# Kernel optimization log

Hardware: AMD Instinct MI355X
Metric: run time of the kernel (lower is better)

The kernel has to match this reference:

```python
import jax, jax.numpy as jnp
import numpy as np

B, C, H, W = 8, 64, 64, 64
IC = max(1, C // 8)  # inter_channels


def setup_inputs() -> dict:
    key = jax.random.key(0)
    ks = jax.random.split(key, 8)
    return {
        "x": jax.random.normal(ks[0], (B, C, H, W), dtype=jnp.float32),
        "theta_w": jax.random.normal(ks[1], (IC, C), dtype=jnp.float32) * 0.05,
        "theta_b": jnp.zeros((IC,), dtype=jnp.float32),
        "phi_w": jax.random.normal(ks[2], (IC, C), dtype=jnp.float32) * 0.05,
        "phi_b": jnp.zeros((IC,), dtype=jnp.float32),
        "g_w": jax.random.normal(ks[3], (C, C), dtype=jnp.float32) * 0.05,
        "g_b": jnp.zeros((C,), dtype=jnp.float32),
        "gamma": jax.random.normal(ks[4], (1,), dtype=jnp.float32),
    }


def reference(x, theta_w, theta_b, phi_w, phi_b, g_w, g_b, gamma):
    b, c, h, w = x.shape
    n = h * w
    xf = x.reshape(b, c, n)  # flatten spatial
    # 1x1 convs == per-pixel channel matmuls
    theta = jnp.einsum('ic,bcn->bin', theta_w, xf) + theta_b[None, :, None]  # [b, IC, n]
    phi = jnp.einsum('ic,bcn->bin', phi_w, xf) + phi_b[None, :, None]        # [b, IC, n]
    g = jnp.einsum('oc,bcn->bon', g_w, xf) + g_b[None, :, None]              # [b, C, n]
    # attn[b, q, k] = theta_q . phi_k, softmax over keys
    attn = jax.nn.softmax(jnp.einsum('biq,bik->bqk', theta, phi), axis=-1)   # [b, n, n]
    # out = g @ attn^T  (torch: bmm(g, attn.transpose(1,2)))
    out = jnp.einsum('bck,bqk->bcq', g, attn).reshape(b, c, h, w)
    return x + gamma[0] * out
```

## Files before the change

### kernel.cpp

```cpp
#include <hip/hip_runtime.h>
#include <cstddef>
#include <cstdint>


#define Bb 8
#define Cc 64
#define NN 4096
#define IC 8
#define VSTR 72
#define XSTR 72

typedef __attribute__((ext_vector_type(8)))  short bf16x8;
typedef __attribute__((ext_vector_type(16))) float f32x16;
typedef unsigned short ushort_t;
typedef unsigned int   uint_t;

#define LOG2E 1.4426950408889634f

static __device__ __forceinline__ uint_t f2bf(float x) {
    union { float f; uint_t u; } v; v.f = x;
    uint_t r = v.u + 0x7FFF + ((v.u >> 16) & 1);
    return r >> 16;
}
static __device__ __forceinline__ float bf2f(ushort_t u) {
    union { uint_t u; float f; } v; v.u = ((uint_t)u) << 16;
    return v.f;
}
static __device__ __forceinline__ float fexp2(float x) {
#if __has_builtin(__builtin_amdgcn_exp2f)
    return __builtin_amdgcn_exp2f(x);
#else
    return exp2f(x);
#endif
}
static __device__ __forceinline__ uint_t fbits(float x) {
    union { float f; uint_t u; } v; v.f = x; return v.u;
}
static __device__ __forceinline__ uint_t packbf(float e, float o) {
#if __has_builtin(__builtin_amdgcn_perm)
    return __builtin_amdgcn_perm(fbits(o), fbits(e), 0x07060302u);
#else
    return (fbits(e) >> 16) | (fbits(o) & 0xFFFF0000u);
#endif
}

union U4B { uint4 u; bf16x8 v; };

__global__ __launch_bounds__(256) void p1_kernel(
    const float* __restrict__ x,
    const float* __restrict__ theta_w, const float* __restrict__ theta_b,
    const float* __restrict__ phi_w,   const float* __restrict__ phi_b,
    const float* __restrict__ g_w,     const float* __restrict__ g_b,
    ushort_t* __restrict__ xbf, ushort_t* __restrict__ Wbf, float* __restrict__ biasf)
{
    const int t = threadIdx.x;
    const int bid = blockIdx.x;
    if (bid < 512) {
        __shared__ float Xt[64 * 68];
        const int b  = bid >> 6;
        const int nt = (bid & 63) * 64;
        const int c = t >> 2, nsg = t & 3;
        const float* xs = x + ((size_t)(b * 64 + c)) * NN + nt + nsg * 16;
        #pragma unroll
        for (int i = 0; i < 4; i++) {
            float4 v = ((const float4*)xs)[i];
            *(float4*)(Xt + c * 68 + nsg * 16 + i * 4) = v;
        }
        __syncthreads();
        const int n = t & 63, cs = t >> 6;
        uint_t wv[8];
        #pragma unroll
        for (int i = 0; i < 8; i++) {
            float e0 = Xt[(cs * 16 + 2 * i + 0) * 68 + n];
            float e1 = Xt[(cs * 16 + 2 * i + 1) * 68 + n];
            wv[i] = f2bf(e0) | (f2bf(e1) << 16);
        }
        ushort_t* dst = xbf + ((size_t)(b * NN + nt + n)) * 64 + cs * 16;
        *(uint4*)dst       = make_uint4(wv[0], wv[1], wv[2], wv[3]);
        *(uint4*)(dst + 8) = make_uint4(wv[4], wv[5], wv[6], wv[7]);
    } else {
        for (int i = t; i < 96 * 64; i += 256) {
            int row = i >> 6, c = i & 63;
            float v;
            if (row < 64)      v = g_w[row * 64 + c];
            else if (row < 72) v = theta_w[(row - 64) * 64 + c] * LOG2E;
            else if (row < 80) v = phi_w[(row - 72) * 64 + c];
            else               v = 0.0f;
            Wbf[i] = (ushort_t)f2bf(v);
        }
        if (t < 96) {
            float bv = (t < 64) ? g_b[t]
                     : (t < 72) ? theta_b[t - 64] * LOG2E
                     : (t < 80) ? phi_b[t - 72] : 0.0f;
            biasf[t] = bv;
        }
    }
}

__global__ __launch_bounds__(256) void p2_kernel(
    const ushort_t* __restrict__ xbf, const ushort_t* __restrict__ Wbf,
    const float* __restrict__ biasf,
    ushort_t* __restrict__ Qw, ushort_t* __restrict__ Kw, ushort_t* __restrict__ Vt)
{
    __shared__ ushort_t Xs[128 * XSTR];
    __shared__ float bs[96];

    const int t = threadIdx.x;
    const int lane = t & 63, w = t >> 6;
    const int l31 = lane & 31, hi = lane >> 5;
    const int b  = blockIdx.x >> 5;
    const int n0 = (blockIdx.x & 31) * 128;

    {
        const int n = t >> 1, h = t & 1;
        const ushort_t* src = xbf + ((size_t)(b * NN + n0 + n)) * 64 + h * 32;
        #pragma unroll
        for (int i = 0; i < 4; i++) {
            uint4 v = ((const uint4*)src)[i];
            *(uint4*)(Xs + n * XSTR + h * 32 + i * 8) = v;
        }
    }
    if (t < 96) bs[t] = biasf[t];
    __syncthreads();

    bf16x8 af[3][4];
    #pragma unroll
    for (int mt = 0; mt < 3; mt++)
        #pragma unroll
        for (int kc = 0; kc < 4; kc++)
            af[mt][kc] = *(const bf16x8*)(Wbf + (size_t)(mt * 32 + l31) * 64 + kc * 16 + hi * 8);

    f32x16 ac0 = {}, ac1 = {}, ac2 = {};
    #pragma unroll
    for (int kc = 0; kc < 4; kc++) {
        bf16x8 bv = *(const bf16x8*)(Xs + (w * 32 + l31) * XSTR + kc * 16 + hi * 8);
        ac0 = __builtin_amdgcn_mfma_f32_32x32x16_bf16(af[0][kc], bv, ac0, 0, 0, 0);
        ac1 = __builtin_amdgcn_mfma_f32_32x32x16_bf16(af[1][kc], bv, ac1, 0, 0, 0);
        ac2 = __builtin_amdgcn_mfma_f32_32x32x16_bf16(af[2][kc], bv, ac2, 0, 0, 0);
    }

    const int nw = n0 + w * 32;
    const int sig = ((l31 >> 3) & 1) * 16 + ((l31 >> 2) & 1) * 8 + ((l31 >> 4) & 1) * 4 + (l31 & 3);

    #pragma unroll
    for (int reg = 0; reg < 16; reg++) {
        int m = reg >> 2, r = reg & 3;
        {
            int ch = 4 * hi + 8 * m + r;
            float val = ac0[reg] + bs[ch];
            Vt[((size_t)(b * 64 + ch)) * NN + nw + sig] = (ushort_t)f2bf(val);
        }
        {
            int ch = 32 + 4 * hi + 8 * m + r;
            float val = ac1[reg] + bs[ch];
            Vt[((size_t)(b * 64 + ch)) * NN + nw + sig] = (ushort_t)f2bf(val);
        }
    }
    {
        float q0 = ac2[0] + bs[64 + 4 * hi + 0];
        float q1 = ac2[1] + bs[64 + 4 * hi + 1];
        float q2 = ac2[2] + bs[64 + 4 * hi + 2];
        float q3 = ac2[3] + bs[64 + 4 * hi + 3];
        uint2 qp = make_uint2(f2bf(q0) | (f2bf(q1) << 16), f2bf(q2) | (f2bf(q3) << 16));
        *(uint2*)(Qw + ((size_t)(b * NN) + nw + l31) * 8 + hi * 4) = qp;
        float p0 = ac2[4] + bs[72 + 4 * hi + 0];
        float p1 = ac2[5] + bs[72 + 4 * hi + 1];
        float p2 = ac2[6] + bs[72 + 4 * hi + 2];
        float p3 = ac2[7] + bs[72 + 4 * hi + 3];
        uint2 kp = make_uint2(f2bf(p0) | (f2bf(p1) << 16), f2bf(p2) | (f2bf(p3) << 16));
        *(uint2*)(Kw + ((size_t)(b * NN) + nw + l31) * 8 + hi * 4) = kp;
    }
}

template <int FIN>
__global__ __launch_bounds__(256) void attn_kernel(
    const ushort_t* __restrict__ Qw, const ushort_t* __restrict__ Kw,
    const ushort_t* __restrict__ Vt,
    ushort_t* __restrict__ P, float* __restrict__ L, int nsplit,
    const float* __restrict__ x, const float* __restrict__ gamma,
    float* __restrict__ out)
{
    __shared__ ushort_t Vs[64 * VSTR];

    const int t = threadIdx.x;
    const int lane = t & 63, w = t >> 6;
    const int l31 = lane & 31, hi = lane >> 5;

    int bid = blockIdx.x;
    const int qt = bid & 31;
    const int b  = (bid >> 5) & 7;
    const int s  = bid >> 8;
    const int q0 = qt * 128 + w * 32;
    const int keys = NN / nsplit;
    const int k0 = s * keys;
    const int ntiles = keys / 64;

    const ushort_t* Kb = Kw + (size_t)b * NN * 8;
    const ushort_t* Vb = Vt + (size_t)b * 64 * NN;

    bf16x8 qf = {};
    if (hi == 0)
        qf = *(const bf16x8*)(Qw + ((size_t)b * NN + q0 + l31) * 8);

    const int vch = t >> 2, vsg = t & 3;
    const ushort_t* vsrc = Vb + (size_t)vch * NN + k0 + vsg * 16;

    uint4 vc0 = *(const uint4*)(vsrc);
    uint4 vc1 = *(const uint4*)(vsrc + 8);
    uint4 kc0 = {}, kc1 = {};
    if (hi == 0) {
        kc0 = *(const uint4*)(Kb + (size_t)(k0 + l31) * 8);
        kc1 = *(const uint4*)(Kb + (size_t)(k0 + 32 + l31) * 8);
    }

    f32x16 acc0 = {}, acc1 = {};
    float lsum = 0.0f;
    const f32x16 zf = {};

    for (int tt = 0; tt < ntiles; ++tt) {
        __syncthreads();
        *(uint4*)(Vs + vch * VSTR + vsg * 16)     = vc0;
        *(uint4*)(Vs + vch * VSTR + vsg * 16 + 8) = vc1;
        __syncthreads();

        uint4 vn0 = {}, vn1 = {}, kn0 = {}, kn1 = {};
        if (tt + 1 < ntiles) {
            const ushort_t* vs2 = vsrc + (size_t)(tt + 1) * 64;
            vn0 = *(const uint4*)(vs2);
            vn1 = *(const uint4*)(vs2 + 8);
            if (hi == 0) {
                kn0 = *(const uint4*)(Kb + (size_t)(k0 + (tt + 1) * 64 + l31) * 8);
                kn1 = *(const uint4*)(Kb + (size_t)(k0 + (tt + 1) * 64 + 32 + l31) * 8);
            }
        }

        U4B ka0, ka1; ka0.u = kc0; ka1.u = kc1;
        f32x16 S0 = __builtin_amdgcn_mfma_f32_32x32x16_bf16(ka0.v, qf, zf, 0, 0, 0);
        f32x16 S1 = __builtin_amdgcn_mfma_f32_32x32x16_bf16(ka1.v, qf, zf, 0, 0, 0);

        float p0[16], p1[16];
        #pragma unroll
        for (int i = 0; i < 16; i++) { p0[i] = fexp2(S0[i]); }
        #pragma unroll
        for (int i = 0; i < 16; i++) { p1[i] = fexp2(S1[i]); }
        #pragma unroll
        for (int i = 0; i < 16; i++) { lsum += p0[i]; lsum += p1[i]; }

        uint_t pk0[8], pk1[8];
        #pragma unroll
        for (int m = 0; m < 4; m++) {
            #pragma unroll
            for (int rp = 0; rp < 2; rp++) {
                pk0[m * 2 + rp] = packbf(p0[m * 4 + 2 * rp], p0[m * 4 + 2 * rp + 1]);
                pk1[m * 2 + rp] = packbf(p1[m * 4 + 2 * rp], p1[m * 4 + 2 * rp + 1]);
            }
        }

        #pragma unroll
        for (int kf = 0; kf < 2; kf++) {
            #pragma unroll
            for (int c = 0; c < 2; c++) {
                U4B bu;
                if (kf == 0) bu.u = make_uint4(pk0[c * 2], pk0[c * 2 + 1], pk0[(c + 2) * 2], pk0[(c + 2) * 2 + 1]);
                else         bu.u = make_uint4(pk1[c * 2], pk1[c * 2 + 1], pk1[(c + 2) * 2], pk1[(c + 2) * 2 + 1]);
                bf16x8 av0 = *(const bf16x8*)(Vs + (0 * 32 + l31) * VSTR + kf * 32 + c * 16 + hi * 8);
                bf16x8 av1 = *(const bf16x8*)(Vs + (1 * 32 + l31) * VSTR + kf * 32 + c * 16 + hi * 8);
                acc0 = __builtin_amdgcn_mfma_f32_32x32x16_bf16(av0, bu.v, acc0, 0, 0, 0);
                acc1 = __builtin_amdgcn_mfma_f32_32x32x16_bf16(av1, bu.v, acc1, 0, 0, 0);
            }
        }

        vc0 = vn0; vc1 = vn1; kc0 = kn0; kc1 = kn1;
    }

    float ltot = lsum + __shfl_xor(lsum, 32);

    if (!FIN) {
        ushort_t* Pb = P + ((size_t)(s * Bb + b) * 64) * NN;
        #pragma unroll
        for (int reg = 0; reg < 16; reg++) {
            int m = reg >> 2, r = reg & 3;
            int ch0 = 4 * hi + 8 * m + r;
            Pb[(size_t)ch0 * NN + q0 + l31]        = (ushort_t)f2bf(acc0[reg]);
            Pb[(size_t)(ch0 + 32) * NN + q0 + l31] = (ushort_t)f2bf(acc1[reg]);
        }
        if (lane < 32)
            L[(size_t)(s * Bb + b) * NN + q0 + lane] = ltot;
    } else {
        const float gm = gamma[0];
        const float inv = 1.0f / ltot;
        #pragma unroll
        for (int reg = 0; reg < 16; reg++) {
            int m = reg >> 2, r = reg & 3;
            int ch0 = 4 * hi + 8 * m + r;
            size_t i0 = ((size_t)(b * 64 + ch0)) * NN + q0 + l31;
            size_t i1 = ((size_t)(b * 64 + ch0 + 32)) * NN + q0 + l31;
            out[i0] = x[i0] + gm * acc0[reg] * inv;
            out[i1] = x[i1] + gm * acc1[reg] * inv;
        }
    }
}

__global__ __launch_bounds__(256) void combine_kernel(
    const ushort_t* __restrict__ P, const float* __restrict__ L,
    const float* __restrict__ x, const float* __restrict__ gamma,
    float* __restrict__ out, int nsplit)
{
    const int T = blockIdx.x * 256 + threadIdx.x;
    const int q = T & (NN - 1);
    const int r2 = T >> 12;
    const int b = r2 & 7;
    const int cg = r2 >> 3;

    float ls = 0.0f;
    for (int s = 0; s < nsplit; s++)
        ls += L[(size_t)(s * Bb + b) * NN + q];

    float a[16];
    #pragma unroll
    for (int j = 0; j < 16; j++) a[j] = 0.0f;
    for (int s = 0; s < nsplit; s++) {
        const ushort_t* Pb = P + ((size_t)(s * Bb + b) * 64 + cg * 16) * NN + q;
        #pragma unroll
        for (int j = 0; j < 16; j++)
            a[j] += bf2f(Pb[(size_t)j * NN]);
    }

    const float inv = 1.0f / ls;
    const float gm = gamma[0];
    #pragma unroll
    for (int j = 0; j < 16; j++) {
        size_t idx = ((size_t)(b * 64 + cg * 16 + j)) * NN + q;
        out[idx] = x[idx] + gm * a[j] * inv;
    }
}

extern "C" void kernel_launch(void* const* d_in, const int* in_sizes, int n_in,
                              void* d_out, int out_size, void* d_ws, size_t ws_size,
                              hipStream_t stream)
{
    const float* x       = (const float*)d_in[0];
    const float* theta_w = (const float*)d_in[1];
    const float* theta_b = (const float*)d_in[2];
    const float* phi_w   = (const float*)d_in[3];
    const float* phi_b   = (const float*)d_in[4];
    const float* g_w     = (const float*)d_in[5];
    const float* g_b     = (const float*)d_in[6];
    const float* gamma   = (const float*)d_in[7];
    float* out = (float*)d_out;

    char* p = (char*)d_ws;
    ushort_t* Qw  = (ushort_t*)p;  p += (size_t)Bb * NN * 8 * 2;
    ushort_t* Kw  = (ushort_t*)p;  p += (size_t)Bb * NN * 8 * 2;
    ushort_t* Vt  = (ushort_t*)p;  p += (size_t)Bb * 64 * NN * 2;
    ushort_t* xbf = (ushort_t*)p;  p += (size_t)Bb * NN * 64 * 2;
    ushort_t* Wbf = (ushort_t*)p;  p += 96 * 64 * 2;
    float*    biasf = (float*)p;   p += 96 * 4 + 128;
    char*     pbase = p;
    const size_t base_bytes  = (size_t)(pbase - (char*)d_ws);
    const size_t split_bytes = (size_t)Bb * 64 * NN * 2 + (size_t)Bb * NN * 4;

    int ns = 1;
    const int cands[3] = {4, 2, 1};
    for (int i = 0; i < 3; i++)
        if (base_bytes + (size_t)cands[i] * split_bytes <= ws_size) { ns = cands[i]; break; }

    ushort_t* P = (ushort_t*)pbase;
    float*    L = (float*)(pbase + (size_t)ns * Bb * 64 * NN * 2);

    p1_kernel<<<513, 256, 0, stream>>>(x, theta_w, theta_b, phi_w, phi_b, g_w, g_b,
                                       xbf, Wbf, biasf);
    p2_kernel<<<Bb * 32, 256, 0, stream>>>(xbf, Wbf, biasf, Qw, Kw, Vt);

    if (ns > 1) {
        attn_kernel<0><<<ns * Bb * 32, 256, 0, stream>>>(Qw, Kw, Vt, P, L, ns,
                                                         nullptr, nullptr, nullptr);
        combine_kernel<<<(Bb * NN * 4) / 256, 256, 0, stream>>>(P, L, x, gamma, out, ns);
    } else {
        attn_kernel<1><<<Bb * 32, 256, 0, stream>>>(Qw, Kw, Vt, P, L, 1, x, gamma, out);
    }
}
```

Before: 57.94 us.

## Double-buffer V tiles with 128-key steps and vectorize combine kernel

The attention kernel now processes 128 keys per iteration, keeps two LDS buffers for V, and prefetches two tiles ahead. This cuts the barriers per tile from two to one and lets global loads overlap the MFMA work. The split count becomes a template parameter so the loop bounds are fixed at compile time. The combine kernel handles 8 queries per thread with 16-byte loads and stores, and its grid shrinks to 128 blocks. This costs more LDS and registers per block, and the smaller combine grid may not fill the GPU.

```diff
diff --git a/kernel.cpp b/kernel.cpp
--- a/kernel.cpp
+++ b/kernel.cpp
@@ -7,7 +7,7 @@
 #define Cc 64
 #define NN 4096
 #define IC 8
-#define VSTR 72
+#define VSTR 136
 #define XSTR 72
 
 typedef __attribute__((ext_vector_type(8)))  short bf16x8;
@@ -22,9 +22,8 @@
     uint_t r = v.u + 0x7FFF + ((v.u >> 16) & 1);
     return r >> 16;
 }
-static __device__ __forceinline__ float bf2f(ushort_t u) {
-    union { uint_t u; float f; } v; v.u = ((uint_t)u) << 16;
-    return v.f;
+static __device__ __forceinline__ float bitsf(uint_t u) {
+    union { uint_t u; float f; } v; v.u = u; return v.f;
 }
 static __device__ __forceinline__ float fexp2(float x) {
 #if __has_builtin(__builtin_amdgcn_exp2f)
@@ -172,15 +171,17 @@
     }
 }
 
-template <int FIN>
+template <int FIN, int NSPLIT>
 __global__ __launch_bounds__(256) void attn_kernel(
     const ushort_t* __restrict__ Qw, const ushort_t* __restrict__ Kw,
     const ushort_t* __restrict__ Vt,
-    ushort_t* __restrict__ P, float* __restrict__ L, int nsplit,
+    ushort_t* __restrict__ P, float* __restrict__ L,
     const float* __restrict__ x, const float* __restrict__ gamma,
     float* __restrict__ out)
 {
-    __shared__ ushort_t Vs[64 * VSTR];
+    constexpr int KEYS = NN / NSPLIT;
+    constexpr int NT = KEYS / 128;
+    __shared__ ushort_t Vs[2][64][VSTR];
 
     const int t = threadIdx.x;
     const int lane = t & 63, w = t >> 6;
@@ -191,9 +192,7 @@
     const int b  = (bid >> 5) & 7;
     const int s  = bid >> 8;
     const int q0 = qt * 128 + w * 32;
-    const int keys = NN / nsplit;
-    const int k0 = s * keys;
-    const int ntiles = keys / 64;
+    const int k0 = s * KEYS;
 
     const ushort_t* Kb = Kw + (size_t)b * NN * 8;
     const ushort_t* Vb = Vt + (size_t)b * 64 * NN;
@@ -203,74 +202,108 @@
         qf = *(const bf16x8*)(Qw + ((size_t)b * NN + q0 + l31) * 8);
 
     const int vch = t >> 2, vsg = t & 3;
-    const ushort_t* vsrc = Vb + (size_t)vch * NN + k0 + vsg * 16;
-
-    uint4 vc0 = *(const uint4*)(vsrc);
-    uint4 vc1 = *(const uint4*)(vsrc + 8);
-    uint4 kc0 = {}, kc1 = {};
+    const ushort_t* vsrc = Vb + (size_t)vch * NN + k0 + vsg * 32;
+
+    uint4 vA[4];
+    uint4 kcur[4] = {make_uint4(0,0,0,0), make_uint4(0,0,0,0),
+                     make_uint4(0,0,0,0), make_uint4(0,0,0,0)};
+    uint4 kA[4]   = {make_uint4(0,0,0,0), make_uint4(0,0,0,0),
+                     make_uint4(0,0,0,0), make_uint4(0,0,0,0)};
+
+    #pragma unroll
+    for (int i = 0; i < 4; i++) vA[i] = *(const uint4*)(vsrc + i * 8);
     if (hi == 0) {
-        kc0 = *(const uint4*)(Kb + (size_t)(k0 + l31) * 8);
-        kc1 = *(const uint4*)(Kb + (size_t)(k0 + 32 + l31) * 8);
-    }
+        #pragma unroll
+        for (int kf = 0; kf < 4; kf++)
+            kcur[kf] = *(const uint4*)(Kb + (size_t)(k0 + kf * 32 + l31) * 8);
+    }
+    #pragma unroll
+    for (int i = 0; i < 4; i++)
+        *(uint4*)(&Vs[0][vch][vsg * 32 + i * 8]) = vA[i];
+    if (NT > 1) {
+        #pragma unroll
+        for (int i = 0; i < 4; i++) vA[i] = *(const uint4*)(vsrc + 128 + i * 8);
+        if (hi == 0) {
+            #pragma unroll
+            for (int kf = 0; kf < 4; kf++)
+                kA[kf] = *(const uint4*)(Kb + (size_t)(k0 + 128 + kf * 32 + l31) * 8);
+        }
+    }
+    __syncthreads();
 
     f32x16 acc0 = {}, acc1 = {};
     float lsum = 0.0f;
     const f32x16 zf = {};
 
-    for (int tt = 0; tt < ntiles; ++tt) {
+    for (int tt = 0; tt < NT; ++tt) {
+        const int cur = tt & 1;
+        if (tt + 1 < NT) {
+            #pragma unroll
+            for (int i = 0; i < 4; i++)
+                *(uint4*)(&Vs[cur ^ 1][vch][vsg * 32 + i * 8]) = vA[i];
+        }
+        if (tt + 2 < NT) {
+            const ushort_t* v2 = vsrc + (size_t)(tt + 2) * 128;
+            #pragma unroll
+            for (int i = 0; i < 4; i++) vA[i] = *(const uint4*)(v2 + i * 8);
+        }
+
+        #pragma unroll
+        for (int ks = 0; ks < 2; ks++) {
+            U4B ka0, ka1;
+            ka0.u = kcur[2 * ks];
+            ka1.u = kcur[2 * ks + 1];
+            f32x16 S0 = __builtin_amdgcn_mfma_f32_32x32x16_bf16(ka0.v, qf, zf, 0, 0, 0);
+            f32x16 S1 = __builtin_amdgcn_mfma_f32_32x32x16_bf16(ka1.v, qf, zf, 0, 0, 0);
+
+            float p0[16], p1[16];
+            #pragma unroll
+            for (int i = 0; i < 16; i++) p0[i] = fexp2(S0[i]);
+            #pragma unroll
+            for (int i = 0; i < 16; i++) p1[i] = fexp2(S1[i]);
+            #pragma unroll
+            for (int i = 0; i < 16; i++) { lsum += p0[i]; lsum += p1[i]; }
+
+            uint_t pk0[8], pk1[8];
+            #pragma unroll
+            for (int m = 0; m < 4; m++) {
+                #pragma unroll
+                for (int rp = 0; rp < 2; rp++) {
+                    pk0[m * 2 + rp] = packbf(p0[m * 4 + 2 * rp], p0[m * 4 + 2 * rp + 1]);
+                    pk1[m * 2 + rp] = packbf(p1[m * 4 + 2 * rp], p1[m * 4 + 2 * rp + 1]);
+                }
+            }
+
+            #pragma unroll
+            for (int kf = 0; kf < 2; kf++) {
+                #pragma unroll
+                for (int c = 0; c < 2; c++) {
+                    U4B bu;
+                    if (kf == 0) bu.u = make_uint4(pk0[c * 2], pk0[c * 2 + 1],
+                                                   pk0[(c + 2) * 2], pk0[(c + 2) * 2 + 1]);
+                    else         bu.u = make_uint4(pk1[c * 2], pk1[c * 2 + 1],
+                                                   pk1[(c + 2) * 2], pk1[(c + 2) * 2 + 1]);
+                    bf16x8 av0 = *(const bf16x8*)(&Vs[cur][0 * 32 + l31][ks * 64 + kf * 32 + c * 16 + hi * 8]);
+                    bf16x8 av1 = *(const bf16x8*)(&Vs[cur][1 * 32 + l31][ks * 64 + kf * 32 + c * 16 + hi * 8]);
+                    acc0 = __builtin_amdgcn_mfma_f32_32x32x16_bf16(av0, bu.v, acc0, 0, 0, 0);
+                    acc1 = __builtin_amdgcn_mfma_f32_32x32x16_bf16(av1, bu.v, acc1, 0, 0, 0);
+                }
+            }
+        }
+
+        if (tt + 1 < NT) {
+            #pragma unroll
+            for (int kf = 0; kf < 4; kf++) kcur[kf] = kA[kf];
+        }
+        if (tt + 2 < NT) {
+            if (hi == 0) {
+                const ushort_t* kk2 = Kb + (size_t)(k0 + (tt + 2) * 128) * 8;
+                #pragma unroll
+                for (int kf = 0; kf < 4; kf++)
+                    kA[kf] = *(const uint4*)(kk2 + (size_t)(kf * 32 + l31) * 8);
+            }
+        }
         __syncthreads();
-        *(uint4*)(Vs + vch * VSTR + vsg * 16)     = vc0;
-        *(uint4*)(Vs + vch * VSTR + vsg * 16 + 8) = vc1;
-        __syncthreads();
-
-        uint4 vn0 = {}, vn1 = {}, kn0 = {}, kn1 = {};
-        if (tt + 1 < ntiles) {
-            const ushort_t* vs2 = vsrc + (size_t)(tt + 1) * 64;
-            vn0 = *(const uint4*)(vs2);
-            vn1 = *(const uint4*)(vs2 + 8);
-            if (hi == 0) {
-                kn0 = *(const uint4*)(Kb + (size_t)(k0 + (tt + 1) * 64 + l31) * 8);
-                kn1 = *(const uint4*)(Kb + (size_t)(k0 + (tt + 1) * 64 + 32 + l31) * 8);
-            }
-        }
-
-        U4B ka0, ka1; ka0.u = kc0; ka1.u = kc1;
-        f32x16 S0 = __builtin_amdgcn_mfma_f32_32x32x16_bf16(ka0.v, qf, zf, 0, 0, 0);
-        f32x16 S1 = __builtin_amdgcn_mfma_f32_32x32x16_bf16(ka1.v, qf, zf, 0, 0, 0);
-
-        float p0[16], p1[16];
-        #pragma unroll
-        for (int i = 0; i < 16; i++) { p0[i] = fexp2(S0[i]); }
-        #pragma unroll
-        for (int i = 0; i < 16; i++) { p1[i] = fexp2(S1[i]); }
-        #pragma unroll
-        for (int i = 0; i < 16; i++) { lsum += p0[i]; lsum += p1[i]; }
-
-        uint_t pk0[8], pk1[8];
-        #pragma unroll
-        for (int m = 0; m < 4; m++) {
-            #pragma unroll
-            for (int rp = 0; rp < 2; rp++) {
-                pk0[m * 2 + rp] = packbf(p0[m * 4 + 2 * rp], p0[m * 4 + 2 * rp + 1]);
-                pk1[m * 2 + rp] = packbf(p1[m * 4 + 2 * rp], p1[m * 4 + 2 * rp + 1]);
-            }
-        }
-
-        #pragma unroll
-        for (int kf = 0; kf < 2; kf++) {
-            #pragma unroll
-            for (int c = 0; c < 2; c++) {
-                U4B bu;
-                if (kf == 0) bu.u = make_uint4(pk0[c * 2], pk0[c * 2 + 1], pk0[(c + 2) * 2], pk0[(c + 2) * 2 + 1]);
-                else         bu.u = make_uint4(pk1[c * 2], pk1[c * 2 + 1], pk1[(c + 2) * 2], pk1[(c + 2) * 2 + 1]);
-                bf16x8 av0 = *(const bf16x8*)(Vs + (0 * 32 + l31) * VSTR + kf * 32 + c * 16 + hi * 8);
-                bf16x8 av1 = *(const bf16x8*)(Vs + (1 * 32 + l31) * VSTR + kf * 32 + c * 16 + hi * 8);
-                acc0 = __builtin_amdgcn_mfma_f32_32x32x16_bf16(av0, bu.v, acc0, 0, 0, 0);
-                acc1 = __builtin_amdgcn_mfma_f32_32x32x16_bf16(av1, bu.v, acc1, 0, 0, 0);
-            }
-        }
-
-        vc0 = vn0; vc1 = vn1; kc0 = kn0; kc1 = kn1;
     }
 
     float ltot = lsum + __shfl_xor(lsum, 32);
@@ -306,32 +339,64 @@
     const float* __restrict__ x, const float* __restrict__ gamma,
     float* __restrict__ out, int nsplit)
 {
-    const int T = blockIdx.x * 256 + threadIdx.x;
-    const int q = T & (NN - 1);
-    const int r2 = T >> 12;
-    const int b = r2 & 7;
-    const int cg = r2 >> 3;
-
-    float ls = 0.0f;
-    for (int s = 0; s < nsplit; s++)
-        ls += L[(size_t)(s * Bb + b) * NN + q];
-
-    float a[16];
-    #pragma unroll
-    for (int j = 0; j < 16; j++) a[j] = 0.0f;
+    const int g = blockIdx.x * 256 + threadIdx.x;
+    const int qo = g & 511;
+    const int q0 = qo * 8;
+    const int rest = g >> 9;
+    const int b  = rest & 7;
+    const int cg = rest >> 3;
+
+    float ls[8];
+    #pragma unroll
+    for (int j = 0; j < 8; j++) ls[j] = 0.f;
     for (int s = 0; s < nsplit; s++) {
-        const ushort_t* Pb = P + ((size_t)(s * Bb + b) * 64 + cg * 16) * NN + q;
-        #pragma unroll
-        for (int j = 0; j < 16; j++)
-            a[j] += bf2f(Pb[(size_t)j * NN]);
-    }
-
-    const float inv = 1.0f / ls;
+        const float* Lb = L + (size_t)(s * Bb + b) * NN + q0;
+        float4 l0 = *(const float4*)(Lb);
+        float4 l1 = *(const float4*)(Lb + 4);
+        ls[0] += l0.x; ls[1] += l0.y; ls[2] += l0.z; ls[3] += l0.w;
+        ls[4] += l1.x; ls[5] += l1.y; ls[6] += l1.z; ls[7] += l1.w;
+    }
+
+    float a[8][8];
+    #pragma unroll
+    for (int j = 0; j < 8; j++)
+        #pragma unroll
+        for (int k = 0; k < 8; k++) a[j][k] = 0.f;
+
+    for (int s = 0; s < nsplit; s++) {
+        #pragma unroll
+        for (int j = 0; j < 8; j++) {
+            const ushort_t* Pr = P + ((size_t)(s * Bb + b) * 64 + cg * 8 + j) * NN + q0;
+            uint4 pv = *(const uint4*)Pr;
+            uint_t u0 = pv.x, u1 = pv.y, u2 = pv.z, u3 = pv.w;
+            a[j][0] += bitsf(u0 << 16); a[j][1] += bitsf(u0 & 0xFFFF0000u);
+            a[j][2] += bitsf(u1 << 16); a[j][3] += bitsf(u1 & 0xFFFF0000u);
+            a[j][4] += bitsf(u2 << 16); a[j][5] += bitsf(u2 & 0xFFFF0000u);
+            a[j][6] += bitsf(u3 << 16); a[j][7] += bitsf(u3 & 0xFFFF0000u);
+        }
+    }
+
+    float inv[8];
+    #pragma unroll
+    for (int k = 0; k < 8; k++) inv[k] = 1.0f / ls[k];
     const float gm = gamma[0];
-    #pragma unroll
-    for (int j = 0; j < 16; j++) {
-        size_t idx = ((size_t)(b * 64 + cg * 16 + j)) * NN + q;
-        out[idx] = x[idx] + gm * a[j] * inv;
+
+    #pragma unroll
+    for (int j = 0; j < 8; j++) {
+        const size_t ro = ((size_t)(b * 64 + cg * 8 + j)) * NN + q0;
+        float4 x0 = *(const float4*)(x + ro);
+        float4 x1 = *(const float4*)(x + ro + 4);
+        float4 o0, o1;
+        o0.x = x0.x + gm * a[j][0] * inv[0];
+        o0.y = x0.y + gm * a[j][1] * inv[1];
+        o0.z = x0.z + gm * a[j][2] * inv[2];
+        o0.w = x0.w + gm * a[j][3] * inv[3];
+        o1.x = x1.x + gm * a[j][4] * inv[4];
+        o1.y = x1.y + gm * a[j][5] * inv[5];
+        o1.z = x1.z + gm * a[j][6] * inv[6];
+        o1.w = x1.w + gm * a[j][7] * inv[7];
+        *(float4*)(out + ro)     = o0;
+        *(float4*)(out + ro + 4) = o1;
     }
 }
 
@@ -372,11 +437,16 @@
                                        xbf, Wbf, biasf);
     p2_kernel<<<Bb * 32, 256, 0, stream>>>(xbf, Wbf, biasf, Qw, Kw, Vt);
 
-    if (ns > 1) {
-        attn_kernel<0><<<ns * Bb * 32, 256, 0, stream>>>(Qw, Kw, Vt, P, L, ns,
-                                                         nullptr, nullptr, nullptr);
-        combine_kernel<<<(Bb * NN * 4) / 256, 256, 0, stream>>>(P, L, x, gamma, out, ns);
+    if (ns == 4) {
+        attn_kernel<0, 4><<<4 * Bb * 32, 256, 0, stream>>>(Qw, Kw, Vt, P, L,
+                                                           x, gamma, out);
+        combine_kernel<<<128, 256, 0, stream>>>(P, L, x, gamma, out, 4);
+    } else if (ns == 2) {
+        attn_kernel<0, 2><<<2 * Bb * 32, 256, 0, stream>>>(Qw, Kw, Vt, P, L,
+                                                           x, gamma, out);
+        combine_kernel<<<128, 256, 0, stream>>>(P, L, x, gamma, out, 2);
     } else {
-        attn_kernel<1><<<Bb * 32, 256, 0, stream>>>(Qw, Kw, Vt, P, L, 1, x, gamma, out);
-    }
-}
+        attn_kernel<1, 1><<<Bb * 32, 256, 0, stream>>>(Qw, Kw, Vt, P, L,
+                                                       x, gamma, out);
+    }
+}
```

Result: slower. 106.0 us (+82.9%).

## Swizzle V shared tile, vectorize combine, allow 8-way key split

Applied to the files above, without the earlier changes.

Replaces the padded V tile in LDS with an XOR-swizzled 64-wide layout, which reduces LDS footprint and aims to avoid bank conflicts on the MFMA operand reads. The combine kernel is reworked so each thread handles 8 consecutive queries across 8 channels, using 16-byte loads and stores for partial sums, normalizers, x and out. The split candidates now include 8, so more attention blocks can run when workspace allows, at the cost of more partial-result traffic in the combine step.

```diff
diff --git a/kernel.cpp b/kernel.cpp
--- a/kernel.cpp
+++ b/kernel.cpp
@@ -7,7 +7,6 @@
 #define Cc 64
 #define NN 4096
 #define IC 8
-#define VSTR 72
 #define XSTR 72
 
 typedef __attribute__((ext_vector_type(8)))  short bf16x8;
@@ -16,15 +15,15 @@
 typedef unsigned int   uint_t;
 
 #define LOG2E 1.4426950408889634f
+#define VIDX(row, slot) (((row) << 6) + (((slot) ^ ((row) & 7)) << 3))
 
 static __device__ __forceinline__ uint_t f2bf(float x) {
     union { float f; uint_t u; } v; v.f = x;
     uint_t r = v.u + 0x7FFF + ((v.u >> 16) & 1);
     return r >> 16;
 }
-static __device__ __forceinline__ float bf2f(ushort_t u) {
-    union { uint_t u; float f; } v; v.u = ((uint_t)u) << 16;
-    return v.f;
+static __device__ __forceinline__ float bitsf(uint_t u) {
+    union { uint_t u; float f; } v; v.u = u; return v.f;
 }
 static __device__ __forceinline__ float fexp2(float x) {
 #if __has_builtin(__builtin_amdgcn_exp2f)
@@ -180,7 +179,7 @@
     const float* __restrict__ x, const float* __restrict__ gamma,
     float* __restrict__ out)
 {
-    __shared__ ushort_t Vs[64 * VSTR];
+    __shared__ ushort_t Vs[64 * 64];
 
     const int t = threadIdx.x;
     const int lane = t & 63, w = t >> 6;
@@ -204,6 +203,8 @@
 
     const int vch = t >> 2, vsg = t & 3;
     const ushort_t* vsrc = Vb + (size_t)vch * NN + k0 + vsg * 16;
+    const int ws0 = VIDX(vch, 2 * vsg);
+    const int ws1 = VIDX(vch, 2 * vsg + 1);
 
     uint4 vc0 = *(const uint4*)(vsrc);
     uint4 vc1 = *(const uint4*)(vsrc + 8);
@@ -219,8 +220,8 @@
 
     for (int tt = 0; tt < ntiles; ++tt) {
         __syncthreads();
-        *(uint4*)(Vs + vch * VSTR + vsg * 16)     = vc0;
-        *(uint4*)(Vs + vch * VSTR + vsg * 16 + 8) = vc1;
+        *(uint4*)(Vs + ws0) = vc0;
+        *(uint4*)(Vs + ws1) = vc1;
         __syncthreads();
 
         uint4 vn0 = {}, vn1 = {}, kn0 = {}, kn1 = {};
@@ -263,8 +264,9 @@
                 U4B bu;
                 if (kf == 0) bu.u = make_uint4(pk0[c * 2], pk0[c * 2 + 1], pk0[(c + 2) * 2], pk0[(c + 2) * 2 + 1]);
                 else         bu.u = make_uint4(pk1[c * 2], pk1[c * 2 + 1], pk1[(c + 2) * 2], pk1[(c + 2) * 2 + 1]);
-                bf16x8 av0 = *(const bf16x8*)(Vs + (0 * 32 + l31) * VSTR + kf * 32 + c * 16 + hi * 8);
-                bf16x8 av1 = *(const bf16x8*)(Vs + (1 * 32 + l31) * VSTR + kf * 32 + c * 16 + hi * 8);
+                const int slot = kf * 4 + c * 2 + hi;
+                bf16x8 av0 = *(const bf16x8*)(Vs + VIDX(l31, slot));
+                bf16x8 av1 = *(const bf16x8*)(Vs + VIDX(32 + l31, slot));
                 acc0 = __builtin_amdgcn_mfma_f32_32x32x16_bf16(av0, bu.v, acc0, 0, 0, 0);
                 acc1 = __builtin_amdgcn_mfma_f32_32x32x16_bf16(av1, bu.v, acc1, 0, 0, 0);
             }
@@ -306,32 +308,64 @@
     const float* __restrict__ x, const float* __restrict__ gamma,
     float* __restrict__ out, int nsplit)
 {
-    const int T = blockIdx.x * 256 + threadIdx.x;
-    const int q = T & (NN - 1);
-    const int r2 = T >> 12;
-    const int b = r2 & 7;
-    const int cg = r2 >> 3;
-
-    float ls = 0.0f;
-    for (int s = 0; s < nsplit; s++)
-        ls += L[(size_t)(s * Bb + b) * NN + q];
-
-    float a[16];
-    #pragma unroll
-    for (int j = 0; j < 16; j++) a[j] = 0.0f;
+    const int g = blockIdx.x * 256 + threadIdx.x;
+    const int qo = g & 511;
+    const int q0 = qo * 8;
+    const int rest = g >> 9;
+    const int b  = rest & 7;
+    const int cg = rest >> 3;
+
+    float ls[8];
+    #pragma unroll
+    for (int j = 0; j < 8; j++) ls[j] = 0.f;
     for (int s = 0; s < nsplit; s++) {
-        const ushort_t* Pb = P + ((size_t)(s * Bb + b) * 64 + cg * 16) * NN + q;
-        #pragma unroll
-        for (int j = 0; j < 16; j++)
-            a[j] += bf2f(Pb[(size_t)j * NN]);
-    }
-
-    const float inv = 1.0f / ls;
+        const float* Lb = L + (size_t)(s * Bb + b) * NN + q0;
+        float4 l0 = *(const float4*)(Lb);
+        float4 l1 = *(const float4*)(Lb + 4);
+        ls[0] += l0.x; ls[1] += l0.y; ls[2] += l0.z; ls[3] += l0.w;
+        ls[4] += l1.x; ls[5] += l1.y; ls[6] += l1.z; ls[7] += l1.w;
+    }
+
+    float a[8][8];
+    #pragma unroll
+    for (int j = 0; j < 8; j++)
+        #pragma unroll
+        for (int k = 0; k < 8; k++) a[j][k] = 0.f;
+
+    for (int s = 0; s < nsplit; s++) {
+        #pragma unroll
+        for (int j = 0; j < 8; j++) {
+            const ushort_t* Pr = P + ((size_t)(s * Bb + b) * 64 + cg * 8 + j) * NN + q0;
+            uint4 pv = *(const uint4*)Pr;
+            uint_t u0 = pv.x, u1 = pv.y, u2 = pv.z, u3 = pv.w;
+            a[j][0] += bitsf(u0 << 16); a[j][1] += bitsf(u0 & 0xFFFF0000u);
+            a[j][2] += bitsf(u1 << 16); a[j][3] += bitsf(u1 & 0xFFFF0000u);
+            a[j][4] += bitsf(u2 << 16); a[j][5] += bitsf(u2 & 0xFFFF0000u);
+            a[j][6] += bitsf(u3 << 16); a[j][7] += bitsf(u3 & 0xFFFF0000u);
+        }
+    }
+
+    float inv[8];
+    #pragma unroll
+    for (int k = 0; k < 8; k++) inv[k] = 1.0f / ls[k];
     const float gm = gamma[0];
-    #pragma unroll
-    for (int j = 0; j < 16; j++) {
-        size_t idx = ((size_t)(b * 64 + cg * 16 + j)) * NN + q;
-        out[idx] = x[idx] + gm * a[j] * inv;
+
+    #pragma unroll
+    for (int j = 0; j < 8; j++) {
+        const size_t ro = ((size_t)(b * 64 + cg * 8 + j)) * NN + q0;
+        float4 x0 = *(const float4*)(x + ro);
+        float4 x1 = *(const float4*)(x + ro + 4);
+        float4 o0, o1;
+        o0.x = x0.x + gm * a[j][0] * inv[0];
+        o0.y = x0.y + gm * a[j][1] * inv[1];
+        o0.z = x0.z + gm * a[j][2] * inv[2];
+        o0.w = x0.w + gm * a[j][3] * inv[3];
+        o1.x = x1.x + gm * a[j][4] * inv[4];
+        o1.y = x1.y + gm * a[j][5] * inv[5];
+        o1.z = x1.z + gm * a[j][6] * inv[6];
+        o1.w = x1.w + gm * a[j][7] * inv[7];
+        *(float4*)(out + ro)     = o0;
+        *(float4*)(out + ro + 4) = o1;
     }
 }
 
@@ -361,8 +395,8 @@
     const size_t split_bytes = (size_t)Bb * 64 * NN * 2 + (size_t)Bb * NN * 4;
 
     int ns = 1;
-    const int cands[3] = {4, 2, 1};
-    for (int i = 0; i < 3; i++)
+    const int cands[4] = {8, 4, 2, 1};
+    for (int i = 0; i < 4; i++)
         if (base_bytes + (size_t)cands[i] * split_bytes <= ws_size) { ns = cands[i]; break; }
 
     ushort_t* P = (ushort_t*)pbase;
@@ -375,8 +409,9 @@
     if (ns > 1) {
         attn_kernel<0><<<ns * Bb * 32, 256, 0, stream>>>(Qw, Kw, Vt, P, L, ns,
                                                          nullptr, nullptr, nullptr);
-        combine_kernel<<<(Bb * NN * 4) / 256, 256, 0, stream>>>(P, L, x, gamma, out, ns);
+        combine_kernel<<<128, 256, 0, stream>>>(P, L, x, gamma, out, ns);
     } else {
-        attn_kernel<1><<<Bb * 32, 256, 0, stream>>>(Qw, Kw, Vt, P, L, 1, x, gamma, out);
-    }
-}
+        attn_kernel<1><<<Bb * 32, 256, 0, stream>>>(Qw, Kw, Vt, P, L, 1,
+                                                    x, gamma, out);
+    }
+}
```

Result: slower. 81.68 us (+41.0%).
